# Optimization experiments

Hardware: AMD Instinct MI355X
Metric: run time of the kernel (lower is better)

Reference implementation:

```python
import jax, jax.numpy as jnp
import numpy as np

B, T, C = 8, 2048, 1024
HS = 64           # head_size
H = C // HS       # n_head = 16
LORA_R = 32       # per-branch lora rank (A is C x 32*5)
TD_R = 64         # time-decay lora rank


def setup_inputs() -> dict:
    key = jax.random.key(0)
    ks = jax.random.split(key, 20)
    inp = {
        "x": jax.random.normal(ks[0], (B, T, C), jnp.float32),
        "miu_x": jax.random.uniform(ks[1], (1, 1, C), jnp.float32),
        "lambda_": jax.random.uniform(ks[2], (5, 1, 1, C), jnp.float32),
        "A_lora": jax.random.normal(ks[3], (C, LORA_R * 5), jnp.float32) * 0.01,
        "B_lora": jax.random.normal(ks[4], (5, LORA_R, C), jnp.float32) * 0.01,
        "td_miu": -6.0 + 5.0 * jax.random.uniform(ks[5], (1, 1, C), jnp.float32),
        "td_A": jax.random.normal(ks[6], (C, TD_R), jnp.float32) * 0.01,
        "td_B": jax.random.normal(ks[7], (TD_R, C), jnp.float32) * 0.01,
        "u": jax.random.normal(ks[8], (H, HS), jnp.float32) * 0.1,
        "Wr": jax.random.normal(ks[9], (C, C), jnp.float32) * 0.02,
        "Wk": jax.random.normal(ks[10], (C, C), jnp.float32) * 0.02,
        "Wv": jax.random.normal(ks[11], (C, C), jnp.float32) * 0.02,
        "Wg": jax.random.normal(ks[12], (C, C), jnp.float32) * 0.02,
        "Wo": jax.random.normal(ks[13], (C, C), jnp.float32) * 0.02,
        "gn_gamma": jnp.ones((C,), jnp.float32),
        "gn_beta": jnp.zeros((C,), jnp.float32),
    }
    return inp


def _wkv6(r, k, v, w, u):
    """RWKV-6 selective-decay linear attention scan.
    r,k,v,w: (b, h, t, n); u: (h, n). Returns y: (b, h, t, n).
    State update: S = diag(exp(-exp(w_t))) S + k_t^T v_t;
    output: y_t = r_t @ (S + diag-free bonus u*k_t^T v_t)."""
    n = r.shape[-1]
    decay = jnp.exp(-jnp.exp(w))  # (b,h,t,n)

    def per_head(rt, kt, vt, dt, uh):  # (t,n) each, uh (n,)
        def step(S, inp):
            ri, ki, vi, di = inp
            kv = ki[:, None] * vi[None, :]          # (n,n)
            y = ri @ (S + uh[:, None] * kv)          # (n,)
            S = di[:, None] * S + kv
            return S, y
        S0 = jnp.zeros((n, n), rt.dtype)
        _, ys = jax.lax.scan(step, S0, (rt, kt, vt, dt))
        return ys  # (t,n)

    f = jax.vmap(per_head, in_axes=(0, 0, 0, 0, 0))       # heads
    f = jax.vmap(f, in_axes=(0, 0, 0, 0, None))           # batch
    return f(r, k, v, decay, u)


def reference(x, miu_x, lambda_, A_lora, B_lora, td_miu, td_A, td_B, u,
              Wr, Wk, Wv, Wg, Wo, gn_gamma, gn_beta):
    b, t, c = x.shape
    h, n = u.shape

    # time_shift: ZeroPad2d((0,0,1,-1)) -> previous token, zeros at t=0
    x_last = jnp.pad(x, ((0, 0), (1, 0), (0, 0)))[:, :t]
    dxa = x_last - x

    # ddlerp: lerp with static miu_x, then data-dependent LoRA mixing coeffs
    xm = x + dxa * miu_x  # (b,t,c)
    lora_h = jnp.tanh(xm @ A_lora).reshape(b, t, 5, -1)        # (b,t,5,32)
    miu = lambda_ + jnp.einsum('btfi,fic->fbtc', lora_h, B_lora)  # (5,b,t,c)
    xx = x[None] + dxa[None] * miu                             # (5,b,t,c)
    w_in, k_in, v_in, r_in, g_in = xx

    k = k_in @ Wk.T
    v = v_in @ Wv.T
    r = r_in @ Wr.T
    g = jax.nn.silu(g_in @ Wg.T)
    w = td_miu + jnp.tanh(w_in @ td_A) @ td_B  # (b,t,c)

    def to_heads(z):
        return z.reshape(b, t, h, n).transpose(0, 2, 1, 3)  # (b,h,t,n)

    y = _wkv6(to_heads(r), to_heads(k), to_heads(v), to_heads(w), u)
    y = y.transpose(0, 2, 1, 3)  # (b,t,h,n)

    # GroupNorm(n_head groups over C) per token, eps = 1e-5 * n_head
    eps = 1e-5 * h
    mean = y.mean(-1, keepdims=True)
    var = y.var(-1, keepdims=True)
    yn = (y - mean) * jax.lax.rsqrt(var + eps)
    yn = yn * gn_gamma.reshape(h, n) + gn_beta.reshape(h, n)
    yn = yn.reshape(b, t, c)

    return (yn * g) @ Wo.T
```

## Files before the change

kernel.cpp:

```cpp
#include <hip/hip_runtime.h>
#include <hip/hip_bf16.h>
#include <cstdint>

typedef __bf16 bf16_t;
typedef __bf16 bf16x8 __attribute__((ext_vector_type(8)));
typedef float f32x4 __attribute__((ext_vector_type(4)));

#define BB 8
#define TT 2048
#define TC 512
#define TCLOG 9
#define NCHUNK 4
#define MCH (BB*TC)
#define CCH 1024
#define HH 16
#define HSZ 64
#define LR5 160
#define LRP 192
#define TDR 64
#define TDK 128
#define TSUB 64
#define NSC (TC/TSUB)
#define BBHH (BB*HH)
#define LDP 72

#define BM 128
#define BN 128
#define BKK 64

enum { EPI_NONE = 0, EPI_SILU = 1, EPI_TANH = 2, EPI_XX = 3, EPI_WBIAS = 4 };

__device__ __forceinline__ void gload16(const bf16_t* g, bf16_t* l) {
    __builtin_amdgcn_global_load_lds(
        (__attribute__((address_space(1))) void*)(g),
        (__attribute__((address_space(3))) void*)(l), 16, 0, 0);
}

__global__ __launch_bounds__(256) void f2b_kernel(const float* __restrict__ in,
        bf16_t* __restrict__ out, int n) {
    int i = blockIdx.x * 256 + threadIdx.x;
    if (i < n) out[i] = (bf16_t)in[i];
}

__global__ __launch_bounds__(256) void transb_pad(const float* __restrict__ in,
        bf16_t* __restrict__ out, int R, int Cc, int Cp) {
    int i = blockIdx.x * 256 + threadIdx.x;
    if (i >= Cp * R) return;
    int row = i / R, col = i - row * R;
    out[i] = (row < Cc) ? (bf16_t)in[(size_t)col * Cc + row] : (bf16_t)0.f;
}

__global__ __launch_bounds__(256) void bbig_pad(const float* __restrict__ B_lora,
        bf16_t* __restrict__ Bbig) {
    int i = blockIdx.x * 256 + threadIdx.x;
    if (i >= 5 * CCH * LRP) return;
    int row = i / LRP, col = i - row * LRP;
    int f = row >> 10, c = row & (CCH - 1);
    int lo = f * 32;
    float v = 0.f;
    if (col >= lo && col < lo + 32)
        v = B_lora[(size_t)(lo + (col - lo)) * CCH + c];
    Bbig[i] = (bf16_t)v;
}

__global__ __launch_bounds__(256) void tdb2_kernel(const float* __restrict__ td_B,
        bf16_t* __restrict__ tdB2) {
    int i = blockIdx.x * 256 + threadIdx.x;
    if (i >= CCH * TDR) return;
    int n = i >> 6, k = i & 63;
    float f = td_B[(size_t)k * CCH + n];
    bf16_t hi = (bf16_t)f;
    bf16_t lo = (bf16_t)(f - (float)hi);
    tdB2[(size_t)n * TDK + k] = hi;
    tdB2[(size_t)n * TDK + TDR + k] = lo;
}

__global__ __launch_bounds__(256) void xm_kernel(const float* __restrict__ x,
        const float* __restrict__ miu_x, bf16_t* __restrict__ xm,
        bf16_t* __restrict__ xb, bf16_t* __restrict__ dxb, int cOff) {
    long long i = (long long)blockIdx.x * 256 + threadIdx.x;
    int ch = (int)(i & (CCH - 1));
    int btl = (int)(i >> 10);
    int b = btl >> TCLOG, tau = btl & (TC - 1);
    int t = cOff + tau;
    size_t gi = ((size_t)b * TT + t) * CCH + ch;
    float xv = x[gi];
    float xp = (t > 0) ? x[gi - CCH] : 0.f;
    float dx = xp - xv;
    xm[i]  = (bf16_t)(xv + dx * miu_x[ch]);
    xb[i]  = (bf16_t)xv;
    dxb[i] = (bf16_t)dx;
}

struct GJob {
    const bf16_t* A;
    const bf16_t* Bw;
    void* C;
    int N;
    int nbmax;
    int K;
    int ldc;
    int epi;
    int outf32;
    int cmap;
    int dup;
};
struct GJobs { GJob j[5]; };

__global__ __launch_bounds__(256) void gemm_jobs(GJobs jobs,
        const float* __restrict__ lam, const float* __restrict__ tdmiu,
        const bf16_t* __restrict__ xb, const bf16_t* __restrict__ dxb,
        bf16_t* __restrict__ xx5, int cOff) {
    const GJob jb = jobs.j[blockIdx.z];
    const int nbx = gridDim.x;
    int flat = blockIdx.y * nbx + blockIdx.x;
    const int cpx = (nbx * gridDim.y) >> 3;
    flat = (flat & 7) * cpx + (flat >> 3);
    const int bx = flat % nbx, by = flat / nbx;
    int m0, n0;
    if (jb.epi == EPI_XX) { n0 = bx * BN; m0 = by * BM; }
    else                  { m0 = bx * BM; n0 = by * BN; }
    if (n0 >= jb.nbmax) return;
    const int K = jb.K;
    __shared__ __align__(16) bf16_t As[BM * BKK];
    __shared__ __align__(16) bf16_t Bs[BN * BKK];
    const int tid = threadIdx.x;
    const int w = tid >> 6, lane = tid & 63;
    const int wm = (w >> 1) * 64, wn = (w & 1) * 64;
    const int lrow = lane & 15;
    const int kq = (lane >> 4) * 8;
    const int srow = tid >> 3;
    const int sc8 = (tid & 7) * 8;
    const bf16_t* Ab = jb.A + (size_t)m0 * K;
    const bf16_t* Bb = jb.Bw + (size_t)n0 * K;
    f32x4 acc[4][4] = {};
    for (int k0 = 0; k0 < K; k0 += BKK) {
        __syncthreads();
        #pragma unroll
        for (int p = 0; p < 4; ++p) {
            int r = srow + p * 32;
            gload16(Ab + (size_t)r * K + k0 + sc8, &As[(tid + p * 256) * 8]);
            gload16(Bb + (size_t)r * K + k0 + sc8, &Bs[(tid + p * 256) * 8]);
        }
        __syncthreads();
        #pragma unroll
        for (int kk = 0; kk < BKK; kk += 32) {
            bf16x8 af[4], bfr[4];
            #pragma unroll
            for (int mt = 0; mt < 4; ++mt)
                af[mt] = *(const bf16x8*)(&As[(wm + mt * 16 + lrow) * BKK + kk + kq]);
            #pragma unroll
            for (int nt = 0; nt < 4; ++nt)
                bfr[nt] = *(const bf16x8*)(&Bs[(wn + nt * 16 + lrow) * BKK + kk + kq]);
            #pragma unroll
            for (int mt = 0; mt < 4; ++mt)
                #pragma unroll
                for (int nt = 0; nt < 4; ++nt)
                    acc[mt][nt] = __builtin_amdgcn_mfma_f32_16x16x32_bf16(
                        af[mt], bfr[nt], acc[mt][nt], 0, 0, 0);
        }
    }
    const int rbase = (lane >> 4) * 4;
    const int col = lane & 15;
    if (jb.epi == EPI_XX) {
        #pragma unroll
        for (int mt = 0; mt < 4; ++mt)
            #pragma unroll
            for (int nt = 0; nt < 4; ++nt) {
                int n = n0 + wn + nt * 16 + col;
                int f = n >> 10, cch = n & (CCH - 1);
                #pragma unroll
                for (int rg = 0; rg < 4; ++rg) {
                    int m = m0 + wm + mt * 16 + rbase + rg;
                    size_t li = (size_t)m * CCH + cch;
                    float xv = (float)xb[li];
                    float dx = (float)dxb[li];
                    float miu = lam[f * CCH + cch] + acc[mt][nt][rg];
                    xx5[(size_t)(f * MCH + m) * CCH + cch] = (bf16_t)(xv + dx * miu);
                }
            }
        return;
    }
    #pragma unroll
    for (int mt = 0; mt < 4; ++mt) {
        #pragma unroll
        for (int nt = 0; nt < 4; ++nt) {
            int n = n0 + wn + nt * 16 + col;
            if (n >= jb.N) continue;
            #pragma unroll
            for (int rg = 0; rg < 4; ++rg) {
                int m = m0 + wm + mt * 16 + rbase + rg;
                size_t mg = jb.cmap ? ((size_t)(m >> TCLOG) * TT + cOff + (m & (TC - 1)))
                                    : (size_t)m;
                float vv = acc[mt][nt][rg];
                if (jb.epi == EPI_SILU) vv = vv / (1.f + expf(-vv));
                else if (jb.epi == EPI_TANH) vv = tanhf(vv);
                else if (jb.epi == EPI_WBIAS) vv += tdmiu[n];
                if (jb.outf32) {
                    ((float*)jb.C)[mg * jb.ldc + n] = vv;
                } else {
                    bf16_t hv = (bf16_t)vv;
                    ((bf16_t*)jb.C)[mg * jb.ldc + n] = hv;
                    if (jb.dup) ((bf16_t*)jb.C)[mg * jb.ldc + n + TDR] = hv;
                }
            }
        }
    }
}

__global__ __launch_bounds__(64) void wkv_prepsg(const bf16_t* __restrict__ ry,
        const bf16_t* __restrict__ k, const float* __restrict__ w,
        const bf16_t* __restrict__ v, const float* __restrict__ u,
        bf16_t* __restrict__ rrT, bf16_t* __restrict__ ktT,
        float* __restrict__ PL, float* __restrict__ bvec,
        float* __restrict__ Sloc) {
    const int bh = blockIdx.x, sc = blockIdx.y;
    const int b = bh >> 4, h = bh & 15;
    const int j = threadIdx.x;
    const size_t base = ((size_t)b * TC + sc * TSUB) * CCH + h * HSZ + j;
    const size_t tile = ((size_t)bh * NSC + sc) * (TSUB * HSZ);
    const size_t vb = (size_t)bh * NSC + sc;
    __shared__ __align__(16) bf16_t ksT[HSZ * LDP];
    __shared__ __align__(16) bf16_t vtT[HSZ * LDP];
    __shared__ float pls[HSZ];
    const float uj = u[h * HSZ + j];
    float pex = 1.f;
    for (int t = 0; t < TSUB; ++t) {
        size_t idx = base + (size_t)t * CCH;
        float rv = (float)ry[idx], kv = (float)k[idx], wv = w[idx];
        bf16_t vv = v[idx];
        float d = expf(-expf(wv));
        rrT[tile + t * HSZ + j] = (bf16_t)(rv * pex);
        float pinc = pex * d;
        bf16_t ktv = (bf16_t)(kv / pinc);
        ktT[tile + t * HSZ + j] = ktv;
        ksT[j * LDP + t] = ktv;
        vtT[j * LDP + t] = vv;
        float bu = rv * uj * kv;
        #pragma unroll
        for (int off = 1; off < 64; off <<= 1) bu += __shfl_xor(bu, off);
        if (j == 0) bvec[vb * TSUB + t] = bu;
        pex = pinc;
    }
    PL[vb * HSZ + j] = pex;
    pls[j] = pex;
    __syncthreads();
    const int lrow = j & 15, kq = (j >> 4) * 8;
    f32x4 acc[4][4] = {};
    #pragma unroll
    for (int kk = 0; kk < TSUB; kk += 32) {
        bf16x8 af[4], bfr[4];
        #pragma unroll
        for (int mt = 0; mt < 4; ++mt)
            af[mt] = *(const bf16x8*)(&ksT[(mt * 16 + lrow) * LDP + kk + kq]);
        #pragma unroll
        for (int nt = 0; nt < 4; ++nt)
            bfr[nt] = *(const bf16x8*)(&vtT[(nt * 16 + lrow) * LDP + kk + kq]);
        #pragma unroll
        for (int mt = 0; mt < 4; ++mt)
            #pragma unroll
            for (int nt = 0; nt < 4; ++nt)
                acc[mt][nt] = __builtin_amdgcn_mfma_f32_16x16x32_bf16(
                    af[mt], bfr[nt], acc[mt][nt], 0, 0, 0);
    }
    const int rbase = (j >> 4) * 4, col = j & 15;
    #pragma unroll
    for (int mt = 0; mt < 4; ++mt)
        #pragma unroll
        for (int nt = 0; nt < 4; ++nt)
            #pragma unroll
            for (int rg = 0; rg < 4; ++rg) {
                int i = mt * 16 + rbase + rg, n = nt * 16 + col;
                Sloc[tile + i * HSZ + n] = pls[i] * acc[mt][nt][rg];
            }
}

__global__ __launch_bounds__(64) void wkv_combine(const float* __restrict__ Sloc,
        const float* __restrict__ PL, float* __restrict__ S0st,
        float* state, int cOuter) {
    const int bh = blockIdx.x;
    const int j = threadIdx.x;
    float* st = state + (size_t)bh * HSZ * HSZ;
    float S[HSZ];
    if (cOuter > 0) {
        #pragma unroll
        for (int i = 0; i < HSZ; ++i) S[i] = st[i * HSZ + j];
    } else {
        #pragma unroll
        for (int i = 0; i < HSZ; ++i) S[i] = 0.f;
    }
    __shared__ float pls[HSZ];
    for (int sc = 0; sc < NSC; ++sc) {
        const size_t so = ((size_t)bh * NSC + sc) * (HSZ * HSZ);
        pls[j] = PL[((size_t)bh * NSC + sc) * HSZ + j];
        __syncthreads();
        #pragma unroll
        for (int i = 0; i < HSZ; ++i) {
            S0st[so + i * HSZ + j] = S[i];
            S[i] = pls[i] * S[i] + Sloc[so + i * HSZ + j];
        }
        __syncthreads();
    }
    #pragma unroll
    for (int i = 0; i < HSZ; ++i) st[i * HSZ + j] = S[i];
}

__global__ __launch_bounds__(64) void wkv_y(bf16_t* __restrict__ ry,
        const bf16_t* __restrict__ rrT, const bf16_t* __restrict__ ktT,
        const bf16_t* __restrict__ v, const float* __restrict__ S0st,
        const float* __restrict__ bvec) {
    const int bh = blockIdx.x, sc = blockIdx.y;
    const int b = bh >> 4, h = bh & 15;
    const int j = threadIdx.x;
    const size_t tile = ((size_t)bh * NSC + sc) * (TSUB * HSZ);
    const size_t basev = ((size_t)b * TC + sc * TSUB) * CCH + h * HSZ;
    __shared__ __align__(16) bf16_t vtT[HSZ * LDP];
    __shared__ __align__(16) bf16_t s0T[HSZ * LDP];
    __shared__ __align__(16) bf16_t am[TSUB * LDP];
    __shared__ float bl[TSUB];
    for (int s = 0; s < TSUB; ++s)
        vtT[j * LDP + s] = v[basev + (size_t)s * CCH + j];
    for (int i = 0; i < HSZ; ++i)
        s0T[j * LDP + i] = (bf16_t)S0st[tile + i * HSZ + j];
    bl[j] = bvec[((size_t)bh * NSC + sc) * TSUB + j];
    __syncthreads();
    const bf16_t* rrt = rrT + tile;
    const bf16_t* ktt = ktT + tile;
    const int lane = j;
    const int lrow = lane & 15, kq = (lane >> 4) * 8;
    const int rbase = (lane >> 4) * 4, col = lane & 15;
    f32x4 acc[4][4] = {};
    #pragma unroll
    for (int kk = 0; kk < HSZ; kk += 32) {
        bf16x8 af[4], bfr[4];
        #pragma unroll
        for (int mt = 0; mt < 4; ++mt)
            af[mt] = *(const bf16x8*)(rrt + (mt * 16 + lrow) * HSZ + kk + kq);
        #pragma unroll
        for (int nt = 0; nt < 4; ++nt)
            bfr[nt] = *(const bf16x8*)(ktt + (nt * 16 + lrow) * HSZ + kk + kq);
        #pragma unroll
        for (int mt = 0; mt < 4; ++mt)
            #pragma unroll
            for (int nt = 0; nt < 4; ++nt)
                acc[mt][nt] = __builtin_amdgcn_mfma_f32_16x16x32_bf16(
                    af[mt], bfr[nt], acc[mt][nt], 0, 0, 0);
    }
    #pragma unroll
    for (int mt = 0; mt < 4; ++mt)
        #pragma unroll
        for (int nt = 0; nt < 4; ++nt)
            #pragma unroll
            for (int rg = 0; rg < 4; ++rg) {
                int t = mt * 16 + rbase + rg, s = nt * 16 + col;
                float aval = (s < t) ? acc[mt][nt][rg] : ((s == t) ? bl[t] : 0.f);
                am[t * LDP + s] = (bf16_t)aval;
            }
    __syncthreads();
    f32x4 yac[4][4] = {};
    #pragma unroll
    for (int kk = 0; kk < TSUB; kk += 32) {
        bf16x8 af[4], bfr[4];
        #pragma unroll
        for (int mt = 0; mt < 4; ++mt)
            af[mt] = *(const bf16x8*)(&am[(mt * 16 + lrow) * LDP + kk + kq]);
        #pragma unroll
        for (int nt = 0; nt < 4; ++nt)
            bfr[nt] = *(const bf16x8*)(&vtT[(nt * 16 + lrow) * LDP + kk + kq]);
        #pragma unroll
        for (int mt = 0; mt < 4; ++mt)
            #pragma unroll
            for (int nt = 0; nt < 4; ++nt)
                yac[mt][nt] = __builtin_amdgcn_mfma_f32_16x16x32_bf16(
                    af[mt], bfr[nt], yac[mt][nt], 0, 0, 0);
    }
    #pragma unroll
    for (int kk = 0; kk < HSZ; kk += 32) {
        bf16x8 af[4], bfr[4];
        #pragma unroll
        for (int mt = 0; mt < 4; ++mt)
            af[mt] = *(const bf16x8*)(rrt + (mt * 16 + lrow) * HSZ + kk + kq);
        #pragma unroll
        for (int nt = 0; nt < 4; ++nt)
            bfr[nt] = *(const bf16x8*)(&s0T[(nt * 16 + lrow) * LDP + kk + kq]);
        #pragma unroll
        for (int mt = 0; mt < 4; ++mt)
            #pragma unroll
            for (int nt = 0; nt < 4; ++nt)
                yac[mt][nt] = __builtin_amdgcn_mfma_f32_16x16x32_bf16(
                    af[mt], bfr[nt], yac[mt][nt], 0, 0, 0);
    }
    #pragma unroll
    for (int mt = 0; mt < 4; ++mt)
        #pragma unroll
        for (int nt = 0; nt < 4; ++nt)
            #pragma unroll
            for (int rg = 0; rg < 4; ++rg) {
                int t = mt * 16 + rbase + rg, jc = nt * 16 + col;
                ry[basev + (size_t)t * CCH + jc] = (bf16_t)yac[mt][nt][rg];
            }
}

__global__ __launch_bounds__(256) void gn_kernel(bf16_t* yg,
        const float* __restrict__ g_glob, const float* __restrict__ gamma,
        const float* __restrict__ beta, int cOff) {
    int wave = threadIdx.x >> 6, lane = threadIdx.x & 63;
    int gid = blockIdx.x * 4 + wave;
    int h = gid & (HH - 1);
    int ml = gid >> 4;
    int b = ml >> TCLOG, tau = ml & (TC - 1);
    size_t lidx = (size_t)ml * CCH + h * HSZ + lane;
    size_t gidx = ((size_t)b * TT + cOff + tau) * CCH + h * HSZ + lane;
    float val = (float)yg[lidx];
    float s = val, s2 = val * val;
    #pragma unroll
    for (int off = 32; off > 0; off >>= 1) {
        s  += __shfl_xor(s, off);
        s2 += __shfl_xor(s2, off);
    }
    float mean = s * (1.f / HSZ);
    float var  = fmaxf(s2 * (1.f / HSZ) - mean * mean, 0.f);
    float inv  = rsqrtf(var + 1e-5f * HH);
    float yn = (val - mean) * inv * gamma[h * HSZ + lane] + beta[h * HSZ + lane];
    yg[lidx] = (bf16_t)(yn * g_glob[gidx]);
}

extern "C" void kernel_launch(void* const* d_in, const int* in_sizes, int n_in,
                              void* d_out, int out_size, void* d_ws, size_t ws_size,
                              hipStream_t stream) {
    const float* x       = (const float*)d_in[0];
    const float* miu_x   = (const float*)d_in[1];
    const float* lambda_ = (const float*)d_in[2];
    const float* A_lora  = (const float*)d_in[3];
    const float* B_lora  = (const float*)d_in[4];
    const float* td_miu  = (const float*)d_in[5];
    const float* td_A    = (const float*)d_in[6];
    const float* td_B    = (const float*)d_in[7];
    const float* u       = (const float*)d_in[8];
    const float* Wr      = (const float*)d_in[9];
    const float* Wk      = (const float*)d_in[10];
    const float* Wv      = (const float*)d_in[11];
    const float* Wg      = (const float*)d_in[12];
    const float* Wo      = (const float*)d_in[13];
    const float* gamma   = (const float*)d_in[14];
    const float* beta    = (const float*)d_in[15];
    float* out = (float*)d_out;

    char* ws = (char*)d_ws;
    size_t off = 0;
    auto alloc = [&](size_t bytes) {
        char* p = ws + off;
        off += (bytes + 255) & ~(size_t)255;
        return (void*)p;
    };
    const size_t MCC = (size_t)MCH * CCH;
    bf16_t* xx5  = (bf16_t*)alloc(5 * MCC * 2);
    float*  Sloc = (float*)xx5;
    float*  S0st = (float*)(xx5 + 2 * MCC);
    bf16_t* xmb  = xx5 + 4 * MCC;
    bf16_t* kc   = (bf16_t*)alloc(MCC * 2);
    bf16_t* vc   = (bf16_t*)alloc(MCC * 2);
    bf16_t* xb16 = kc;
    bf16_t* dx16 = vc;
    float*  wc   = (float*)alloc(MCC * 4);
    bf16_t* ryc  = (bf16_t*)alloc(MCC * 2);
    bf16_t* rrT  = (bf16_t*)alloc(MCC * 2);
    bf16_t* ktT  = (bf16_t*)alloc(MCC * 2);
    bf16_t* lhcp = (bf16_t*)alloc((size_t)MCH * LRP * 2);
    bf16_t* tdh2 = (bf16_t*)alloc((size_t)MCH * TDK * 2);
    bf16_t* At   = (bf16_t*)alloc((size_t)256 * CCH * 2);
    bf16_t* tdAt = (bf16_t*)alloc((size_t)128 * CCH * 2);
    bf16_t* tdB2 = (bf16_t*)alloc((size_t)CCH * TDK * 2);
    bf16_t* Bbig = (bf16_t*)alloc((size_t)5 * CCH * LRP * 2);
    bf16_t* Wb[5];
    for (int i = 0; i < 5; ++i) Wb[i] = (bf16_t*)alloc((size_t)CCH * CCH * 2);
    float*  state = (float*)alloc((size_t)BBHH * HSZ * HSZ * 4);
    float*  PL    = (float*)alloc((size_t)BBHH * NSC * HSZ * 4);
    float*  bvec  = (float*)alloc((size_t)BBHH * NSC * TSUB * 4);
    (void)ws_size; (void)in_sizes; (void)n_in; (void)out_size;
    bf16_t* Wrb = Wb[0]; bf16_t* Wkb = Wb[1]; bf16_t* Wvb = Wb[2];
    bf16_t* Wgb = Wb[3]; bf16_t* Wob = Wb[4];

    const int WN = CCH * CCH;
    f2b_kernel<<<(WN + 255) / 256, 256, 0, stream>>>(Wr, Wrb, WN);
    f2b_kernel<<<(WN + 255) / 256, 256, 0, stream>>>(Wk, Wkb, WN);
    f2b_kernel<<<(WN + 255) / 256, 256, 0, stream>>>(Wv, Wvb, WN);
    f2b_kernel<<<(WN + 255) / 256, 256, 0, stream>>>(Wg, Wgb, WN);
    f2b_kernel<<<(WN + 255) / 256, 256, 0, stream>>>(Wo, Wob, WN);
    transb_pad<<<(256 * CCH + 255) / 256, 256, 0, stream>>>(A_lora, At, CCH, LR5, 256);
    transb_pad<<<(128 * CCH + 255) / 256, 256, 0, stream>>>(td_A, tdAt, CCH, TDR, 128);
    tdb2_kernel<<<(CCH * TDR + 255) / 256, 256, 0, stream>>>(td_B, tdB2);
    bbig_pad<<<(5 * CCH * LRP + 255) / 256, 256, 0, stream>>>(B_lora, Bbig);

    for (int c = 0; c < NCHUNK; ++c) {
        const int cOff = c * TC;
        xm_kernel<<<MCC / 256, 256, 0, stream>>>(x, miu_x, xmb, xb16, dx16, cOff);
        {
            GJobs J = {};
            J.j[0] = {xmb, At, lhcp, LRP, 256, CCH, LRP, EPI_TANH, 0, 0, 0};
            gemm_jobs<<<dim3(32, 2, 1), 256, 0, stream>>>(J, lambda_, td_miu, xb16, dx16, xx5, cOff);
        }
        {
            GJobs J = {};
            J.j[0] = {lhcp, Bbig, nullptr, 5 * CCH, 5 * CCH, LRP, 0, EPI_XX, 0, 0, 0};
            gemm_jobs<<<dim3(40, 32, 1), 256, 0, stream>>>(J, lambda_, td_miu, xb16, dx16, xx5, cOff);
        }
        {
            GJobs J = {};
            J.j[0] = {xx5 + 1 * MCC, Wkb,  kc,   CCH, CCH, CCH, CCH, EPI_NONE, 0, 0, 0};
            J.j[1] = {xx5 + 2 * MCC, Wvb,  vc,   CCH, CCH, CCH, CCH, EPI_NONE, 0, 0, 0};
            J.j[2] = {xx5 + 3 * MCC, Wrb,  ryc,  CCH, CCH, CCH, CCH, EPI_NONE, 0, 0, 0};
            J.j[3] = {xx5 + 4 * MCC, Wgb,  out,  CCH, CCH, CCH, CCH, EPI_SILU, 1, 1, 0};
            J.j[4] = {xx5 + 0 * MCC, tdAt, tdh2, TDR, 128, CCH, TDK, EPI_TANH, 0, 0, 1};
            gemm_jobs<<<dim3(32, 8, 5), 256, 0, stream>>>(J, lambda_, td_miu, xb16, dx16, xx5, cOff);
        }
        {
            GJobs J = {};
            J.j[0] = {tdh2, tdB2, wc, CCH, CCH, TDK, CCH, EPI_WBIAS, 1, 0, 0};
            gemm_jobs<<<dim3(32, 8, 1), 256, 0, stream>>>(J, lambda_, td_miu, xb16, dx16, xx5, cOff);
        }
        wkv_prepsg<<<dim3(BBHH, NSC), 64, 0, stream>>>(ryc, kc, wc, vc, u,
                                                       rrT, ktT, PL, bvec, Sloc);
        wkv_combine<<<BBHH, 64, 0, stream>>>(Sloc, PL, S0st, state, c);
        wkv_y<<<dim3(BBHH, NSC), 64, 0, stream>>>(ryc, rrT, ktT, vc, S0st, bvec);
        gn_kernel<<<(MCH * HH) / 4, 256, 0, stream>>>(ryc, out, gamma, beta, cOff);
        {
            GJobs J = {};
            J.j[0] = {ryc, Wob, out, CCH, CCH, CCH, CCH, EPI_NONE, 1, 1, 0};
            gemm_jobs<<<dim3(32, 8, 1), 256, 0, stream>>>(J, lambda_, td_miu, xb16, dx16, xx5, cOff);
        }
    }
}
```

Before: 1.399 ms.

## Double-buffer GEMM shared-memory tiles and drop block-index swizzle

The GEMM kernel now stages K-tiles into two shared-memory buffers so the next tile's global-to-LDS loads are issued before computing on the current tile, with one barrier per step instead of two. It also removes the XCD-style block-index remapping and uses plain blockIdx.x/y for m0/n0, swapping the EPI_XX launch grid dimensions to match. This is meant to overlap load latency with MFMA work. In exchange it doubles LDS use, which may reduce occupancy, and losing the swizzle may hurt L2 locality across XCDs.

```diff
diff --git a/kernel.cpp b/kernel.cpp
--- a/kernel.cpp
+++ b/kernel.cpp
@@ -112,18 +112,12 @@
         const bf16_t* __restrict__ xb, const bf16_t* __restrict__ dxb,
         bf16_t* __restrict__ xx5, int cOff) {
     const GJob jb = jobs.j[blockIdx.z];
-    const int nbx = gridDim.x;
-    int flat = blockIdx.y * nbx + blockIdx.x;
-    const int cpx = (nbx * gridDim.y) >> 3;
-    flat = (flat & 7) * cpx + (flat >> 3);
-    const int bx = flat % nbx, by = flat / nbx;
-    int m0, n0;
-    if (jb.epi == EPI_XX) { n0 = bx * BN; m0 = by * BM; }
-    else                  { m0 = bx * BM; n0 = by * BN; }
+    const int m0 = blockIdx.x * BM;
+    const int n0 = blockIdx.y * BN;
     if (n0 >= jb.nbmax) return;
     const int K = jb.K;
-    __shared__ __align__(16) bf16_t As[BM * BKK];
-    __shared__ __align__(16) bf16_t Bs[BN * BKK];
+    __shared__ __align__(16) bf16_t As[2][BM * BKK];
+    __shared__ __align__(16) bf16_t Bs[2][BN * BKK];
     const int tid = threadIdx.x;
     const int w = tid >> 6, lane = tid & 63;
     const int wm = (w >> 1) * 64, wn = (w & 1) * 64;
@@ -134,24 +128,31 @@
     const bf16_t* Ab = jb.A + (size_t)m0 * K;
     const bf16_t* Bb = jb.Bw + (size_t)n0 * K;
     f32x4 acc[4][4] = {};
-    for (int k0 = 0; k0 < K; k0 += BKK) {
-        __syncthreads();
+    const int nsteps = K / BKK;
+
+    auto stage = [&](int buf, int k0) {
         #pragma unroll
         for (int p = 0; p < 4; ++p) {
             int r = srow + p * 32;
-            gload16(Ab + (size_t)r * K + k0 + sc8, &As[(tid + p * 256) * 8]);
-            gload16(Bb + (size_t)r * K + k0 + sc8, &Bs[(tid + p * 256) * 8]);
-        }
-        __syncthreads();
+            gload16(Ab + (size_t)r * K + k0 + sc8, &As[buf][(tid + p * 256) * 8]);
+            gload16(Bb + (size_t)r * K + k0 + sc8, &Bs[buf][(tid + p * 256) * 8]);
+        }
+    };
+
+    stage(0, 0);
+    __syncthreads();
+    int cur = 0;
+    for (int s = 0; s < nsteps; ++s) {
+        if (s + 1 < nsteps) stage(cur ^ 1, (s + 1) * BKK);
         #pragma unroll
         for (int kk = 0; kk < BKK; kk += 32) {
             bf16x8 af[4], bfr[4];
             #pragma unroll
             for (int mt = 0; mt < 4; ++mt)
-                af[mt] = *(const bf16x8*)(&As[(wm + mt * 16 + lrow) * BKK + kk + kq]);
+                af[mt] = *(const bf16x8*)(&As[cur][(wm + mt * 16 + lrow) * BKK + kk + kq]);
             #pragma unroll
             for (int nt = 0; nt < 4; ++nt)
-                bfr[nt] = *(const bf16x8*)(&Bs[(wn + nt * 16 + lrow) * BKK + kk + kq]);
+                bfr[nt] = *(const bf16x8*)(&Bs[cur][(wn + nt * 16 + lrow) * BKK + kk + kq]);
             #pragma unroll
             for (int mt = 0; mt < 4; ++mt)
                 #pragma unroll
@@ -159,6 +160,8 @@
                     acc[mt][nt] = __builtin_amdgcn_mfma_f32_16x16x32_bf16(
                         af[mt], bfr[nt], acc[mt][nt], 0, 0, 0);
         }
+        __syncthreads();
+        cur ^= 1;
     }
     const int rbase = (lane >> 4) * 4;
     const int col = lane & 15;
@@ -503,7 +506,7 @@
         {
             GJobs J = {};
             J.j[0] = {lhcp, Bbig, nullptr, 5 * CCH, 5 * CCH, LRP, 0, EPI_XX, 0, 0, 0};
-            gemm_jobs<<<dim3(40, 32, 1), 256, 0, stream>>>(J, lambda_, td_miu, xb16, dx16, xx5, cOff);
+            gemm_jobs<<<dim3(32, 40, 1), 256, 0, stream>>>(J, lambda_, td_miu, xb16, dx16, xx5, cOff);
         }
         {
             GJobs J = {};
```

Result: faster. 1.349 ms (-3.6%).
